# Kernel tuning notes

Measured on AMD Instinct MI355X. Metric: run time of the kernel, lower is better.

The kernel has to match this reference:

```python
import jax, jax.numpy as jnp
import numpy as np

B, T, N, D, H = 4, 8, 128, 256, 8
DH = D // H
SH_HID = 16
NUM_FEATS = 3
NUM_COEFF = 4  # l=0 (1) + l=1 (3)
Y0_CONST = 0.28209479177387814   # 1/(2*sqrt(pi)), e3nn 'integral' norm
Y1_CONST = 0.4886025119029199    # sqrt(3/(4*pi))


def setup_inputs() -> dict:
    key = jax.random.key(0)
    ks = jax.random.split(key, 16)
    rn = lambda k, shape, s=1.0: jax.random.normal(k, shape, dtype=jnp.float32) * s
    return {
        "x_0": rn(ks[0], (B, T, N, D)),
        "v_0": rn(ks[1], (B, T, N, D)),
        "concatenated_features": rn(ks[2], (B, T, N, D)),
        "q_data": rn(ks[3], (B, T, N, D)),
        "mask": jnp.ones((B, 1, N, 1), dtype=bool),
        "Wq": rn(ks[4], (D, D), 0.02), "bq": jnp.zeros((D,), jnp.float32),
        "Wkv": rn(ks[5], (NUM_FEATS, D, 2 * D), 0.02),
        "bkv": jnp.zeros((NUM_FEATS, 2 * D), jnp.float32),
        "Wo": rn(ks[6], (D, D), 0.02), "bo": jnp.zeros((D,), jnp.float32),
        "feature_weights": rn(ks[7], (NUM_FEATS,), 0.1),
        "attention_denom": jnp.full((H,), float(DH), dtype=jnp.float32),
        "sh_W1": rn(ks[8], (NUM_COEFF, SH_HID), 0.3), "sh_b1": jnp.zeros((SH_HID,), jnp.float32),
        "sh_W2": rn(ks[9], (SH_HID, SH_HID), 0.3), "sh_b2": jnp.zeros((SH_HID,), jnp.float32),
        "sh_W3": rn(ks[10], (SH_HID, H), 0.3), "sh_b3": jnp.zeros((H,), jnp.float32),
    }


def _rope(t, mask, T_, N_):
    # t: [B,H,S,dh]; time-only RoPE, groups of N_ nodes share a timestep. offset=0.
    B_, H_, S, dh = t.shape
    half = dh // 2
    freqs = 1.0 / (1000.0 ** (2.0 * jnp.arange(half, dtype=jnp.float32) / dh))  # [half]
    pos = jnp.repeat(jnp.arange(T_, dtype=jnp.float32), N_)  # [S]
    angle = pos[:, None] * freqs[None, :]  # [S, half]
    mask_seq = jnp.broadcast_to(mask, (B_, T_, N_, 1)).reshape(B_, 1, S, 1)
    cos_t = jnp.where(mask_seq, jnp.cos(angle)[None, None], 1.0)  # [B,1,S,half]
    sin_t = jnp.where(mask_seq, jnp.sin(angle)[None, None], 0.0)
    t1, t2 = t[..., 0::2], t[..., 1::2]
    return jnp.stack([t1 * cos_t - t2 * sin_t, t1 * sin_t + t2 * cos_t], axis=-1).reshape(t.shape)


def _sh_bias(coords, W1, b1, W2, b2, W3, b3):
    # coords: [B,S,3] -> bias [B,H,S,S]
    rel = coords[:, :, None, :] - coords[:, None, :, :]  # [B,S,S,3]
    norm = jnp.sqrt(jnp.sum(rel * rel, axis=-1, keepdims=True))
    u = rel / (norm + 1e-6)
    Y0 = jnp.full(u.shape[:-1] + (1,), Y0_CONST, dtype=u.dtype)
    Y1 = Y1_CONST * u[..., jnp.array([1, 2, 0])]  # e3nn l=1 order (y,z,x)
    sh = jnp.concatenate([Y0, Y1], axis=-1)  # [B,S,S,4]
    h = jax.nn.silu(sh @ W1 + b1)
    h = jax.nn.silu(h @ W2 + b2)
    bias = h @ W3 + b3  # [B,S,S,H]
    return jnp.transpose(bias, (0, 3, 1, 2))


def reference(x_0, v_0, concatenated_features, q_data, mask,
              Wq, bq, Wkv, bkv, Wo, bo, feature_weights, attention_denom,
              sh_W1, sh_b1, sh_W2, sh_b2, sh_W3, sh_b3):
    B_, T_, N_, D_ = q_data.shape
    S = T_ * N_
    H_ = attention_denom.shape[0]
    dh = D_ // H_

    q = (q_data.reshape(B_, S, D_) @ Wq + bq).reshape(B_, S, H_, dh).transpose(0, 2, 1, 3)
    q = _rope(q, mask, T_, N_)

    coords = x_0[..., :3].reshape(B_, S, 3)
    bias = _sh_bias(coords, sh_W1, sh_b1, sh_W2, sh_b2, sh_W3, sh_b3)  # [B,H,S,S]

    key_mask = jnp.broadcast_to(mask, (B_, T_, N_, 1)).reshape(B_, 1, 1, S)
    gates = jax.nn.softmax(feature_weights)

    out_sum = jnp.zeros_like(q)
    for i, feat in enumerate((x_0, v_0, concatenated_features)):
        kv = feat.reshape(B_, S, D_) @ Wkv[i] + bkv[i]  # [B,S,2D]
        k = kv[..., :D_].reshape(B_, S, H_, dh).transpose(0, 2, 1, 3)
        v = kv[..., D_:].reshape(B_, S, H_, dh).transpose(0, 2, 1, 3)
        k = _rope(k, mask, T_, N_)
        scores = jnp.einsum('bhqd,bhkd->bhqk', q, k) / attention_denom[None, :, None, None]
        scores = scores + bias
        scores = jnp.where(key_mask, scores, -1e9)
        attn = jax.nn.softmax(scores, axis=-1)
        out_sum = out_sum + gates[i] * jnp.einsum('bhqk,bhkd->bhqd', attn, v)

    out = out_sum.transpose(0, 2, 1, 3).reshape(B_, S, D_) @ Wo + bo  # [B,S,D]
    return out.reshape(B_ * T_, N_, D_)
```

## Files before the change

kernel.cpp:

```cpp
#include <hip/hip_runtime.h>
#include <hip/hip_bf16.h>
#include <math.h>


typedef __bf16 bf16;
typedef __attribute__((ext_vector_type(8))) __bf16 bf16x8;
typedef __attribute__((ext_vector_type(4))) __bf16 bf16x4;
typedef __attribute__((ext_vector_type(4))) float  f32x4;

#define MFMA16(a,b,c) __builtin_amdgcn_mfma_f32_16x16x32_bf16((a),(b),(c),0,0,0)
#define FRCP(x) __builtin_amdgcn_rcpf(x)

__global__ __launch_bounds__(256) void proj_kernel(
    const float* __restrict__ x0, const float* __restrict__ v0,
    const float* __restrict__ cf, const float* __restrict__ qd,
    const float* __restrict__ Wq, const float* __restrict__ bq,
    const float* __restrict__ Wkv, const float* __restrict__ bkv,
    const float* __restrict__ dn,
    bf16* __restrict__ Qb, bf16* __restrict__ Kb, bf16* __restrict__ Vtb)
{
  const int z  = blockIdx.z;
  const int mt = blockIdx.x;
  const int nt = blockIdx.y;
  if (z == 0 && nt >= 4) return;

  const float* A; const float* W; const float* bias; int ldw;
  if (z == 0){ A = qd; W = Wq; bias = bq; ldw = 256; }
  else {
    A = (z==1) ? x0 : (z==2) ? v0 : cf;
    W = Wkv + (size_t)(z-1)*256*512;
    bias = bkv + (size_t)(z-1)*512;
    ldw = 512;
  }

  __shared__ alignas(16) bf16 lds_a[64*264];
  __shared__ alignas(16) bf16 lds_w[64*264];
  const int t  = threadIdx.x;
  const int n0 = nt*64;

  #pragma unroll
  for (int i=0;i<16;i++){
    int flat = i*256 + t;
    int r = flat >> 6, c4 = flat & 63;
    float4 v = *(const float4*)(A + (size_t)(mt*64 + r)*256 + c4*4);
    bf16* dst = lds_a + r*264 + c4*4;
    dst[0]=(bf16)v.x; dst[1]=(bf16)v.y; dst[2]=(bf16)v.z; dst[3]=(bf16)v.w;
  }
  {
    int c4 = t & 15, kr = t >> 4;
    #pragma unroll
    for (int i=0;i<16;i++){
      int k = kr + i*16;
      float4 v = *(const float4*)(W + (size_t)k*ldw + n0 + c4*4);
      lds_w[(c4*4+0)*264 + k] = (bf16)v.x;
      lds_w[(c4*4+1)*264 + k] = (bf16)v.y;
      lds_w[(c4*4+2)*264 + k] = (bf16)v.z;
      lds_w[(c4*4+3)*264 + k] = (bf16)v.w;
    }
  }
  __syncthreads();

  const int w = t>>6, lane = t&63, lrow = lane&15, g = lane>>4;
  const f32x4 zf = {0.f,0.f,0.f,0.f};
  f32x4 acc[4] = {zf,zf,zf,zf};

  #pragma unroll
  for (int ks=0;ks<8;ks++){
    bf16x8 a = *(const bf16x8*)(lds_a + (w*16+lrow)*264 + ks*32 + g*8);
    #pragma unroll
    for (int n4=0;n4<4;n4++){
      bf16x8 bb = *(const bf16x8*)(lds_w + (n4*16+lrow)*264 + ks*32 + g*8);
      acc[n4] = MFMA16(a, bb, acc[n4]);
    }
  }

  const bool isV = (z>0) && (nt>=4);
  if (!isV){
    const float tpos = (float)((mt & 15) >> 1);
    const float Cln = 0.43172239f;
    float fr_e = __expf(-Cln * (float)(lrow>>1));
    float fr_o = __expf(-Cln * (float)(8 + (lrow>>1)));
    float ae = tpos*fr_e, ao = tpos*fr_o;
    float cs_e = __cosf(ae), sn_e = __sinf(ae);
    float cs_o = __cosf(ao), sn_o = __sinf(ao);
    float rs0 = 1.f, rs1 = 1.f;
    if (z==0){ rs0 = 1.f/dn[(nt*2)&7]; rs1 = 1.f/dn[(nt*2+1)&7]; }

    #pragma unroll
    for (int n4=0;n4<4;n4++){
      int gcol = n0 + n4*16 + lrow;
      float bv = bias[gcol];
      float cs = (n4&1)? cs_o : cs_e;
      float sn = (n4&1)? sn_o : sn_e;
      float rs = (n4>>1)? rs1 : rs0;
      #pragma unroll
      for (int rr=0;rr<4;rr++){
        float v = acc[n4][rr] + bv;
        float p = __shfl_xor(v, 1);
        float o = (lrow&1) ? (p*sn + v*cs) : (v*cs - p*sn);
        o *= rs;
        lds_a[(w*16 + g*4 + rr)*264 + n4*16 + lrow] = (bf16)o;
      }
    }
    int row = lane>>2, c8 = lane&3;
    int srow = mt*64 + w*16 + row;
    int bb = srow>>10, s = srow&1023;
    #pragma unroll
    for (int hh=0; hh<2; hh++){
      bf16x8 val = *(const bf16x8*)(lds_a + (w*16+row)*264 + hh*32 + c8*8);
      int h = (nt*2 + hh)&7;
      bf16* dst = (z==0) ? (Qb + ((size_t)(bb*8+h)*1024 + s)*32 + c8*8)
                         : (Kb + ((size_t)(((z-1)*4+bb)*8+h)*1024 + s)*32 + c8*8);
      *(bf16x8*)dst = val;
    }
  } else {
    #pragma unroll
    for (int n4=0;n4<4;n4++){
      int gcol = n0 + n4*16 + lrow;
      float bv = bias[gcol];
      int hd = gcol - 256; int h = hd>>5, d = hd&31;
      int grow0 = mt*64 + w*16 + g*4;
      int bb = grow0>>10, s0 = grow0&1023;
      int s0p = (s0 & ~31) | (((s0>>2)&3)<<3) | (((s0>>4)&1)<<2);
      bf16x4 pk;
      #pragma unroll
      for (int rr=0;rr<4;rr++) pk[rr] = (bf16)(acc[n4][rr] + bv);
      *(bf16x4*)(Vtb + (((size_t)((z-1)*4+bb)*8 + h)*32 + d)*1024 + s0p) = pk;
    }
  }
}

template<bool PART>
__global__ __launch_bounds__(512) void attn_kernel(
    const bf16* __restrict__ Qb, const bf16* __restrict__ Kb, const bf16* __restrict__ Vtb,
    const float* __restrict__ x0, const float* __restrict__ fw,
    const float* __restrict__ W1, const float* __restrict__ b1,
    const float* __restrict__ W2, const float* __restrict__ b2,
    const float* __restrict__ W3, const float* __restrict__ b3,
    float* __restrict__ osum, float* __restrict__ Pp, float* __restrict__ Lp)
{
  const int bid = blockIdx.x;
  const int xcd = bid & 7;
  const int b   = xcd >> 1;
  int qt, split;
  if (PART){ int r = bid>>3; qt = (xcd&1)*32 + (r&31); split = r>>5; }
  else     { qt = (xcd&1)*32 + (bid>>3); split = 0; }
  const int q0 = qt*16;
  constexpr int KTS = PART ? 8 : 16;
  constexpr int KC  = PART ? 512 : 1024;
  const int kbase = split*512;
  const int t = threadIdx.x, w = t>>6, lane = t&63, lrow = lane&15, g = lane>>4;

  __shared__ float ckA[KC][3];
  __shared__ float biasT[8*64*17];

  bf16x8 w1f, w2f, w3f;
  #pragma unroll
  for (int j=0;j<8;j++){
    w1f[j] = (g==0 && j<4)   ? (bf16)W1[j*16 + lrow]       : (bf16)0.f;
    w2f[j] = (j<4)           ? (bf16)W2[(4*g+j)*16 + lrow] : (bf16)0.f;
    w3f[j] = (j<4 && lrow<8) ? (bf16)W3[(4*g+j)*8 + lrow]  : (bf16)0.f;
  }
  float b1r[4], b2r[4], b3r[4];
  #pragma unroll
  for (int rr=0;rr<4;rr++){
    b1r[rr] = b1[g*4+rr];
    b2r[rr] = b2[g*4+rr];
    b3r[rr] = (g<2) ? b3[g*4+rr] : 0.f;
  }

  bf16x8 qf = *(const bf16x8*)(Qb + (((size_t)(b*8+w)*1024) + q0 + lrow)*32 + g*8);

  #pragma unroll
  for (int u=0; u<KC/512; u++){
    int key = u*512 + t;
    const float* src = x0 + ((size_t)b*1024 + kbase + key)*256;
    ckA[key][0] = src[0]; ckA[key][1] = src[1]; ckA[key][2] = src[2];
  }
  const float* qsrc = x0 + ((size_t)b*1024 + q0 + lrow)*256;
  const float cqx = qsrc[0], cqy = qsrc[1], cqz = qsrc[2];
  __syncthreads();

  float l_run[3] = {0.f,0.f,0.f};
  const f32x4 zf = {0.f,0.f,0.f,0.f};
  f32x4 acc[3][2];
  #pragma unroll
  for (int i=0;i<3;i++){ acc[i][0] = zf; acc[i][1] = zf; }

  for (int kt=0;kt<KTS;kt++){
    const int k0 = kt*64;
    const int kg = kbase + k0;

    #pragma unroll
    for (int m8=0;m8<8;m8++){
      const int m = w*8 + m8;
      float rx = cqx - ckA[k0+m][0];
      float ry = cqy - ckA[k0+m][1];
      float rz = cqz - ckA[k0+m][2];
      float inv = FRCP(__builtin_amdgcn_sqrtf(rx*rx+ry*ry+rz*rz) + 1e-6f);
      bf16x8 shf;
      #pragma unroll
      for (int j=0;j<8;j++) shf[j] = (bf16)0.f;
      if (g==0){
        shf[0] = (bf16)0.28209479177387814f;
        shf[1] = (bf16)(0.4886025119029199f*ry*inv);
        shf[2] = (bf16)(0.4886025119029199f*rz*inv);
        shf[3] = (bf16)(0.4886025119029199f*rx*inv);
      }
      f32x4 c1 = MFMA16(w1f, shf, zf);
      bf16x8 h1f;
      #pragma unroll
      for (int rr=0;rr<4;rr++){
        float hv = c1[rr] + b1r[rr];
        hv = hv * FRCP(1.f + __expf(-hv));
        bf16 hb = (bf16)hv;
        h1f[rr] = hb; h1f[rr+4] = hb;
      }
      f32x4 c2 = MFMA16(w2f, h1f, zf);
      bf16x8 h2f;
      #pragma unroll
      for (int rr=0;rr<4;rr++){
        float hv = c2[rr] + b2r[rr];
        hv = hv * FRCP(1.f + __expf(-hv));
        bf16 hb = (bf16)hv;
        h2f[rr] = hb; h2f[rr+4] = hb;
      }
      f32x4 c3 = MFMA16(w3f, h2f, zf);
      if (g < 2){
        #pragma unroll
        for (int rr=0;rr<4;rr++)
          biasT[((g*4+rr)*64 + m)*17 + lrow] = c3[rr] + b3r[rr];
      }
    }
    __syncthreads();

    float bias_r[4][4];
    #pragma unroll
    for (int k16=0;k16<4;k16++)
      #pragma unroll
      for (int rr=0;rr<4;rr++)
        bias_r[k16][rr] = biasT[(w*64 + k16*16 + g*4 + rr)*17 + lrow];

    #pragma unroll
    for (int i=0;i<3;i++){
      const bf16* Kbase = Kb + ((size_t)(i*4+b)*8 + w)*1024*32;
      float p[4][4];
      float ls = 0.f;
      #pragma unroll
      for (int k16=0;k16<4;k16++){
        bf16x8 kf = *(const bf16x8*)(Kbase + (size_t)(kg + k16*16 + lrow)*32 + g*8);
        f32x4 sc = MFMA16(kf, qf, zf);
        #pragma unroll
        for (int rr=0;rr<4;rr++){
          float pv = __expf(sc[rr] + bias_r[k16][rr]);
          p[k16][rr] = pv;
          ls += pv;
        }
      }
      l_run[i] += ls;
      bf16x8 pf0, pf1;
      #pragma unroll
      for (int j=0;j<8;j++){
        pf0[j] = (bf16)p[(j>>2)][j&3];
        pf1[j] = (bf16)p[2+(j>>2)][j&3];
      }
      const bf16* Vbase = Vtb + ((size_t)(i*4+b)*8 + w)*32*1024;
      #pragma unroll
      for (int dt=0;dt<2;dt++){
        bf16x8 vf0 = *(const bf16x8*)(Vbase + (size_t)(dt*16+lrow)*1024 + kg      + g*8);
        bf16x8 vf1 = *(const bf16x8*)(Vbase + (size_t)(dt*16+lrow)*1024 + kg + 32 + g*8);
        acc[i][dt] = MFMA16(vf0, pf0, acc[i][dt]);
        acc[i][dt] = MFMA16(vf1, pf1, acc[i][dt]);
      }
    }
    __syncthreads();
  }

  if (PART){
    #pragma unroll
    for (int i=0;i<3;i++){
      float l = l_run[i];
      l += __shfl_xor(l, 16);
      l += __shfl_xor(l, 32);
      if (lane < 16)
        Lp[((size_t)(i*2+split)*4+b)*8192 + w*1024 + q0 + lrow] = l;
      #pragma unroll
      for (int dt=0;dt<2;dt++)
        *(f32x4*)(Pp + (((size_t)(i*2+split)*4 + b)*1024 + q0 + lrow)*256
                     + w*32 + dt*16 + g*4) = acc[i][dt];
    }
  } else {
    float f0=fw[0], f1=fw[1], f2=fw[2];
    float fm = fmaxf(f0, fmaxf(f1,f2));
    float e0=__expf(f0-fm), e1=__expf(f1-fm), e2=__expf(f2-fm);
    float ei = FRCP(e0+e1+e2);
    float gate[3] = {e0*ei, e1*ei, e2*ei};
    float linv[3];
    #pragma unroll
    for (int i=0;i<3;i++){
      float l = l_run[i];
      l += __shfl_xor(l, 16);
      l += __shfl_xor(l, 32);
      linv[i] = gate[i]*FRCP(l);
    }
    #pragma unroll
    for (int dt=0;dt<2;dt++){
      f32x4 o;
      #pragma unroll
      for (int rr=0;rr<4;rr++)
        o[rr] = acc[0][dt][rr]*linv[0] + acc[1][dt][rr]*linv[1] + acc[2][dt][rr]*linv[2];
      *(f32x4*)(osum + ((size_t)b*1024 + q0 + lrow)*256 + w*32 + dt*16 + g*4) = o;
    }
  }
}

__global__ __launch_bounds__(256) void combine_kernel(
    const float* __restrict__ Pp, const float* __restrict__ Lp,
    const float* __restrict__ fw, float* __restrict__ osum)
{
  int idx  = blockIdx.x*256 + threadIdx.x;
  int col4 = idx & 63;
  int row  = idx >> 6;
  int b = row >> 10, q = row & 1023;
  int h = col4 >> 3;
  float f0=fw[0], f1=fw[1], f2=fw[2];
  float fm = fmaxf(f0, fmaxf(f1,f2));
  float e0=__expf(f0-fm), e1=__expf(f1-fm), e2=__expf(f2-fm);
  float ei = 1.f/(e0+e1+e2);
  float gate[3] = {e0*ei, e1*ei, e2*ei};
  f32x4 o = {0.f,0.f,0.f,0.f};
  #pragma unroll
  for (int i=0;i<3;i++){
    f32x4 a = ((const f32x4*)Pp)[(((size_t)(i*2+0)*4 + b)*1024 + q)*64 + col4];
    f32x4 c = ((const f32x4*)Pp)[(((size_t)(i*2+1)*4 + b)*1024 + q)*64 + col4];
    float l = Lp[((size_t)(i*2+0)*4+b)*8192 + h*1024 + q]
            + Lp[((size_t)(i*2+1)*4+b)*8192 + h*1024 + q];
    float s = gate[i]/l;
    #pragma unroll
    for (int rr=0;rr<4;rr++) o[rr] += (a[rr]+c[rr])*s;
  }
  ((f32x4*)osum)[idx] = o;
}

__global__ __launch_bounds__(256) void oproj_kernel(
    const float* __restrict__ As, const float* __restrict__ Wo,
    const float* __restrict__ bo, float* __restrict__ out)
{
  const int mt = blockIdx.x, nt = blockIdx.y;
  __shared__ alignas(16) bf16 lds_a[64*264];
  __shared__ alignas(16) bf16 lds_w[64*264];
  const int t = threadIdx.x;
  const int n0 = nt*64;
  #pragma unroll
  for (int i=0;i<16;i++){
    int flat = i*256 + t;
    int r = flat >> 6, c4 = flat & 63;
    float4 v = *(const float4*)(As + (size_t)(mt*64 + r)*256 + c4*4);
    bf16* dst = lds_a + r*264 + c4*4;
    dst[0]=(bf16)v.x; dst[1]=(bf16)v.y; dst[2]=(bf16)v.z; dst[3]=(bf16)v.w;
  }
  {
    int c4 = t & 15, kr = t >> 4;
    #pragma unroll
    for (int i=0;i<16;i++){
      int k = kr + i*16;
      float4 v = *(const float4*)(Wo + (size_t)k*256 + n0 + c4*4);
      lds_w[(c4*4+0)*264 + k] = (bf16)v.x;
      lds_w[(c4*4+1)*264 + k] = (bf16)v.y;
      lds_w[(c4*4+2)*264 + k] = (bf16)v.z;
      lds_w[(c4*4+3)*264 + k] = (bf16)v.w;
    }
  }
  __syncthreads();
  const int w = t>>6, lane = t&63, lrow = lane&15, g = lane>>4;
  const f32x4 zf = {0.f,0.f,0.f,0.f};
  f32x4 acc[4] = {zf,zf,zf,zf};
  #pragma unroll
  for (int ks=0;ks<8;ks++){
    bf16x8 a = *(const bf16x8*)(lds_a + (w*16+lrow)*264 + ks*32 + g*8);
    #pragma unroll
    for (int n4=0;n4<4;n4++){
      bf16x8 bb = *(const bf16x8*)(lds_w + (n4*16+lrow)*264 + ks*32 + g*8);
      acc[n4] = MFMA16(a, bb, acc[n4]);
    }
  }
  #pragma unroll
  for (int n4=0;n4<4;n4++){
    int gcol = n0 + n4*16 + lrow;
    float bv = bo[gcol];
    #pragma unroll
    for (int rr=0;rr<4;rr++){
      int grow = mt*64 + w*16 + g*4 + rr;
      out[(size_t)grow*256 + gcol] = acc[n4][rr] + bv;
    }
  }
}

extern "C" void kernel_launch(void* const* d_in, const int* in_sizes, int n_in,
                              void* d_out, int out_size, void* d_ws, size_t ws_size,
                              hipStream_t stream)
{
  (void)in_sizes; (void)n_in; (void)out_size;
  const float* x0 = (const float*)d_in[0];
  const float* v0 = (const float*)d_in[1];
  const float* cf = (const float*)d_in[2];
  const float* qd = (const float*)d_in[3];
  const float* Wq = (const float*)d_in[5];
  const float* bq = (const float*)d_in[6];
  const float* Wkv= (const float*)d_in[7];
  const float* bkv= (const float*)d_in[8];
  const float* Wo = (const float*)d_in[9];
  const float* bo = (const float*)d_in[10];
  const float* fw = (const float*)d_in[11];
  const float* dn = (const float*)d_in[12];
  const float* W1 = (const float*)d_in[13];
  const float* b1 = (const float*)d_in[14];
  const float* W2 = (const float*)d_in[15];
  const float* b2 = (const float*)d_in[16];
  const float* W3 = (const float*)d_in[17];
  const float* b3 = (const float*)d_in[18];

  const size_t nQ = (size_t)4*8*1024*32;
  const size_t nK = (size_t)3*4*8*1024*32;
  bf16*  Qb   = (bf16*)d_ws;
  bf16*  Kb   = Qb + nQ;
  bf16*  Vtb  = Kb + nK;
  float* osum = (float*)(Vtb + nK);
  float* Pp   = osum + (size_t)4*1024*256;
  float* Lp   = Pp + (size_t)3*2*4*1024*256;
  const size_t need_part = (nQ + 2*nK)*2
                         + ((size_t)4*1024*256 + (size_t)3*2*4*1024*256 + (size_t)3*2*4*8*1024)*4;
  float* outp = (float*)d_out;

  hipLaunchKernelGGL(proj_kernel, dim3(64,8,4), dim3(256), 0, stream,
                     x0, v0, cf, qd, Wq, bq, Wkv, bkv, dn, Qb, Kb, Vtb);
  if (ws_size >= need_part){
    hipLaunchKernelGGL((attn_kernel<true>), dim3(512), dim3(512), 0, stream,
                       Qb, Kb, Vtb, x0, fw, W1,b1,W2,b2,W3,b3, osum, Pp, Lp);
    hipLaunchKernelGGL(combine_kernel, dim3(1024), dim3(256), 0, stream,
                       Pp, Lp, fw, osum);
  } else {
    hipLaunchKernelGGL((attn_kernel<false>), dim3(256), dim3(512), 0, stream,
                       Qb, Kb, Vtb, x0, fw, W1,b1,W2,b2,W3,b3, osum, Pp, Lp);
  }
  hipLaunchKernelGGL(oproj_kernel, dim3(64,4), dim3(256), 0, stream,
                     osum, Wo, bo, outp);
}
```

Before: 260.3 us.

## Merge key-split attention into one 1024-thread block and rework projection grid

The attention key split now runs inside a single 1024-thread block, with two wave groups each covering half the keys. The partial results are merged through shared memory, which removes the Pp/Lp global partial buffers and the separate combine kernel launch. The projection kernel drops its idle z=0 blocks with a compact 16x28 grid. Each projection block now loops over 4 M-tiles while reusing the staged weight tile, and A is read directly from global memory into registers instead of through LDS. Risks include lower occupancy from the 1024-thread blocks and larger shared memory use, fewer blocks in the projection kernel, and uncoalesced direct loads of A.

Result: slower. 278.4 us (+7.0%).

```diff
diff --git a/kernel.cpp b/kernel.cpp
--- a/kernel.cpp
+++ b/kernel.cpp
@@ -19,10 +19,10 @@
     const float* __restrict__ dn,
     bf16* __restrict__ Qb, bf16* __restrict__ Kb, bf16* __restrict__ Vtb)
 {
-  const int z  = blockIdx.z;
-  const int mt = blockIdx.x;
-  const int nt = blockIdx.y;
-  if (z == 0 && nt >= 4) return;
+  const int mtc = blockIdx.x;
+  const int znt = blockIdx.y;
+  int z, nt;
+  if (znt < 4){ z = 0; nt = znt; } else { z = 1 + ((znt-4)>>3); nt = (znt-4)&7; }
 
   const float* A; const float* W; const float* bias; int ldw;
   if (z == 0){ A = qd; W = Wq; bias = bq; ldw = 256; }
@@ -33,19 +33,11 @@
     ldw = 512;
   }
 
-  __shared__ alignas(16) bf16 lds_a[64*264];
   __shared__ alignas(16) bf16 lds_w[64*264];
+  __shared__ alignas(16) bf16 ostg[4][1152];
   const int t  = threadIdx.x;
   const int n0 = nt*64;
 
-  #pragma unroll
-  for (int i=0;i<16;i++){
-    int flat = i*256 + t;
-    int r = flat >> 6, c4 = flat & 63;
-    float4 v = *(const float4*)(A + (size_t)(mt*64 + r)*256 + c4*4);
-    bf16* dst = lds_a + r*264 + c4*4;
-    dst[0]=(bf16)v.x; dst[1]=(bf16)v.y; dst[2]=(bf16)v.z; dst[3]=(bf16)v.w;
-  }
   {
     int c4 = t & 15, kr = t >> 4;
     #pragma unroll
@@ -62,97 +54,104 @@
 
   const int w = t>>6, lane = t&63, lrow = lane&15, g = lane>>4;
   const f32x4 zf = {0.f,0.f,0.f,0.f};
-  f32x4 acc[4] = {zf,zf,zf,zf};
-
-  #pragma unroll
-  for (int ks=0;ks<8;ks++){
-    bf16x8 a = *(const bf16x8*)(lds_a + (w*16+lrow)*264 + ks*32 + g*8);
-    #pragma unroll
-    for (int n4=0;n4<4;n4++){
-      bf16x8 bb = *(const bf16x8*)(lds_w + (n4*16+lrow)*264 + ks*32 + g*8);
-      acc[n4] = MFMA16(a, bb, acc[n4]);
-    }
-  }
-
   const bool isV = (z>0) && (nt>=4);
-  if (!isV){
-    const float tpos = (float)((mt & 15) >> 1);
-    const float Cln = 0.43172239f;
-    float fr_e = __expf(-Cln * (float)(lrow>>1));
-    float fr_o = __expf(-Cln * (float)(8 + (lrow>>1)));
-    float ae = tpos*fr_e, ao = tpos*fr_o;
-    float cs_e = __cosf(ae), sn_e = __sinf(ae);
-    float cs_o = __cosf(ao), sn_o = __sinf(ao);
-    float rs0 = 1.f, rs1 = 1.f;
-    if (z==0){ rs0 = 1.f/dn[(nt*2)&7]; rs1 = 1.f/dn[(nt*2+1)&7]; }
-
-    #pragma unroll
-    for (int n4=0;n4<4;n4++){
-      int gcol = n0 + n4*16 + lrow;
-      float bv = bias[gcol];
-      float cs = (n4&1)? cs_o : cs_e;
-      float sn = (n4&1)? sn_o : sn_e;
-      float rs = (n4>>1)? rs1 : rs0;
-      #pragma unroll
-      for (int rr=0;rr<4;rr++){
-        float v = acc[n4][rr] + bv;
-        float p = __shfl_xor(v, 1);
-        float o = (lrow&1) ? (p*sn + v*cs) : (v*cs - p*sn);
-        o *= rs;
-        lds_a[(w*16 + g*4 + rr)*264 + n4*16 + lrow] = (bf16)o;
-      }
-    }
-    int row = lane>>2, c8 = lane&3;
-    int srow = mt*64 + w*16 + row;
-    int bb = srow>>10, s = srow&1023;
-    #pragma unroll
-    for (int hh=0; hh<2; hh++){
-      bf16x8 val = *(const bf16x8*)(lds_a + (w*16+row)*264 + hh*32 + c8*8);
-      int h = (nt*2 + hh)&7;
-      bf16* dst = (z==0) ? (Qb + ((size_t)(bb*8+h)*1024 + s)*32 + c8*8)
-                         : (Kb + ((size_t)(((z-1)*4+bb)*8+h)*1024 + s)*32 + c8*8);
-      *(bf16x8*)dst = val;
-    }
-  } else {
-    #pragma unroll
-    for (int n4=0;n4<4;n4++){
-      int gcol = n0 + n4*16 + lrow;
-      float bv = bias[gcol];
-      int hd = gcol - 256; int h = hd>>5, d = hd&31;
-      int grow0 = mt*64 + w*16 + g*4;
-      int bb = grow0>>10, s0 = grow0&1023;
-      int s0p = (s0 & ~31) | (((s0>>2)&3)<<3) | (((s0>>4)&1)<<2);
-      bf16x4 pk;
-      #pragma unroll
-      for (int rr=0;rr<4;rr++) pk[rr] = (bf16)(acc[n4][rr] + bv);
-      *(bf16x4*)(Vtb + (((size_t)((z-1)*4+bb)*8 + h)*32 + d)*1024 + s0p) = pk;
+
+  const float Cln = 0.43172239f;
+  const float fr_e = __expf(-Cln * (float)(lrow>>1));
+  const float fr_o = __expf(-Cln * (float)(8 + (lrow>>1)));
+  float rs0 = 1.f, rs1 = 1.f;
+  if (z==0){ rs0 = 1.f/dn[(nt*2)&7]; rs1 = 1.f/dn[(nt*2+1)&7]; }
+
+  for (int mi=0; mi<4; mi++){
+    const int mt = mtc*4 + mi;
+    const float* Arow = A + (size_t)(mt*64 + w*16 + lrow)*256;
+
+    f32x4 acc[4] = {zf,zf,zf,zf};
+    #pragma unroll
+    for (int ks=0;ks<8;ks++){
+      float4 a0 = *(const float4*)(Arow + ks*32 + g*8);
+      float4 a1 = *(const float4*)(Arow + ks*32 + g*8 + 4);
+      bf16x8 af = {(bf16)a0.x,(bf16)a0.y,(bf16)a0.z,(bf16)a0.w,
+                   (bf16)a1.x,(bf16)a1.y,(bf16)a1.z,(bf16)a1.w};
+      #pragma unroll
+      for (int n4=0;n4<4;n4++){
+        bf16x8 bb = *(const bf16x8*)(lds_w + (n4*16+lrow)*264 + ks*32 + g*8);
+        acc[n4] = MFMA16(af, bb, acc[n4]);
+      }
+    }
+
+    if (!isV){
+      const float tpos = (float)((mt>>1)&7);
+      float ae = tpos*fr_e, ao = tpos*fr_o;
+      float cs_e = __cosf(ae), sn_e = __sinf(ae);
+      float cs_o = __cosf(ao), sn_o = __sinf(ao);
+      #pragma unroll
+      for (int n4=0;n4<4;n4++){
+        int gcol = n0 + n4*16 + lrow;
+        float bv = bias[gcol];
+        float cs = (n4&1)? cs_o : cs_e;
+        float sn = (n4&1)? sn_o : sn_e;
+        float rs = (n4>>1)? rs1 : rs0;
+        #pragma unroll
+        for (int rr=0;rr<4;rr++){
+          float v = acc[n4][rr] + bv;
+          float p = __shfl_xor(v, 1);
+          float o = (lrow&1) ? (p*sn + v*cs) : (v*cs - p*sn);
+          o *= rs;
+          ostg[w][(g*4+rr)*72 + n4*16 + lrow] = (bf16)o;
+        }
+      }
+      asm volatile("s_waitcnt lgkmcnt(0)" ::: "memory");
+      int row = lane>>2, c8 = lane&3;
+      int srow = mt*64 + w*16 + row;
+      int bb = srow>>10, s = srow&1023;
+      #pragma unroll
+      for (int hh=0; hh<2; hh++){
+        bf16x8 val = *(const bf16x8*)(ostg[w] + row*72 + hh*32 + c8*8);
+        int h = (nt*2 + hh)&7;
+        bf16* dst = (z==0) ? (Qb + ((size_t)(bb*8+h)*1024 + s)*32 + c8*8)
+                           : (Kb + ((size_t)(((z-1)*4+bb)*8+h)*1024 + s)*32 + c8*8);
+        *(bf16x8*)dst = val;
+      }
+    } else {
+      #pragma unroll
+      for (int n4=0;n4<4;n4++){
+        int gcol = n0 + n4*16 + lrow;
+        float bv = bias[gcol];
+        int hd = gcol - 256; int h = hd>>5, d = hd&31;
+        int grow0 = mt*64 + w*16 + g*4;
+        int bb = grow0>>10, s0 = grow0&1023;
+        int s0p = (s0 & ~31) | (((s0>>2)&3)<<3) | (((s0>>4)&1)<<2);
+        bf16x4 pk;
+        #pragma unroll
+        for (int rr=0;rr<4;rr++) pk[rr] = (bf16)(acc[n4][rr] + bv);
+        *(bf16x4*)(Vtb + (((size_t)((z-1)*4+bb)*8 + h)*32 + d)*1024 + s0p) = pk;
+      }
     }
   }
 }
 
-template<bool PART>
-__global__ __launch_bounds__(512) void attn_kernel(
+__global__ __launch_bounds__(1024) void attn_kernel(
     const bf16* __restrict__ Qb, const bf16* __restrict__ Kb, const bf16* __restrict__ Vtb,
     const float* __restrict__ x0, const float* __restrict__ fw,
     const float* __restrict__ W1, const float* __restrict__ b1,
     const float* __restrict__ W2, const float* __restrict__ b2,
     const float* __restrict__ W3, const float* __restrict__ b3,
-    float* __restrict__ osum, float* __restrict__ Pp, float* __restrict__ Lp)
+    float* __restrict__ osum)
 {
   const int bid = blockIdx.x;
   const int xcd = bid & 7;
   const int b   = xcd >> 1;
-  int qt, split;
-  if (PART){ int r = bid>>3; qt = (xcd&1)*32 + (r&31); split = r>>5; }
-  else     { qt = (xcd&1)*32 + (bid>>3); split = 0; }
-  const int q0 = qt*16;
-  constexpr int KTS = PART ? 8 : 16;
-  constexpr int KC  = PART ? 512 : 1024;
+  const int qt  = (xcd & 1)*32 + (bid >> 3);
+  const int q0  = qt*16;
+  const int t = threadIdx.x;
+  const int w16 = t>>6, split = w16>>3, w = w16&7;
+  const int lane = t&63, lrow = lane&15, g = lane>>4;
   const int kbase = split*512;
-  const int t = threadIdx.x, w = t>>6, lane = t&63, lrow = lane&15, g = lane>>4;
-
-  __shared__ float ckA[KC][3];
-  __shared__ float biasT[8*64*17];
+
+  __shared__ float smem[20480];
+  float* ckA = smem;
+  float* bT  = smem + 3072 + split*8704;
 
   bf16x8 w1f, w2f, w3f;
   #pragma unroll
@@ -171,15 +170,12 @@
 
   bf16x8 qf = *(const bf16x8*)(Qb + (((size_t)(b*8+w)*1024) + q0 + lrow)*32 + g*8);
 
-  #pragma unroll
-  for (int u=0; u<KC/512; u++){
-    int key = u*512 + t;
-    const float* src = x0 + ((size_t)b*1024 + kbase + key)*256;
-    ckA[key][0] = src[0]; ckA[key][1] = src[1]; ckA[key][2] = src[2];
-  }
-  const float* qsrc = x0 + ((size_t)b*1024 + q0 + lrow)*256;
-  const float cqx = qsrc[0], cqy = qsrc[1], cqz = qsrc[2];
+  {
+    const float* src = x0 + ((size_t)b*1024 + t)*256;
+    ckA[t*3+0] = src[0]; ckA[t*3+1] = src[1]; ckA[t*3+2] = src[2];
+  }
   __syncthreads();
+  const float cqx = ckA[(q0+lrow)*3+0], cqy = ckA[(q0+lrow)*3+1], cqz = ckA[(q0+lrow)*3+2];
 
   float l_run[3] = {0.f,0.f,0.f};
   const f32x4 zf = {0.f,0.f,0.f,0.f};
@@ -187,16 +183,15 @@
   #pragma unroll
   for (int i=0;i<3;i++){ acc[i][0] = zf; acc[i][1] = zf; }
 
-  for (int kt=0;kt<KTS;kt++){
-    const int k0 = kt*64;
-    const int kg = kbase + k0;
+  for (int kt=0;kt<8;kt++){
+    const int kg = kbase + kt*64;
 
     #pragma unroll
     for (int m8=0;m8<8;m8++){
       const int m = w*8 + m8;
-      float rx = cqx - ckA[k0+m][0];
-      float ry = cqy - ckA[k0+m][1];
-      float rz = cqz - ckA[k0+m][2];
+      float rx = cqx - ckA[(kg+m)*3+0];
+      float ry = cqy - ckA[(kg+m)*3+1];
+      float rz = cqz - ckA[(kg+m)*3+2];
       float inv = FRCP(__builtin_amdgcn_sqrtf(rx*rx+ry*ry+rz*rz) + 1e-6f);
       bf16x8 shf;
       #pragma unroll
@@ -229,7 +224,7 @@
       if (g < 2){
         #pragma unroll
         for (int rr=0;rr<4;rr++)
-          biasT[((g*4+rr)*64 + m)*17 + lrow] = c3[rr] + b3r[rr];
+          bT[((g*4+rr)*64 + m)*17 + lrow] = c3[rr] + b3r[rr];
       }
     }
     __syncthreads();
@@ -239,7 +234,7 @@
     for (int k16=0;k16<4;k16++)
       #pragma unroll
       for (int rr=0;rr<4;rr++)
-        bias_r[k16][rr] = biasT[(w*64 + k16*16 + g*4 + rr)*17 + lrow];
+        bias_r[k16][rr] = bT[(w*64 + k16*16 + g*4 + rr)*17 + lrow];
 
     #pragma unroll
     for (int i=0;i<3;i++){
@@ -276,20 +271,28 @@
     __syncthreads();
   }
 
-  if (PART){
+  if (split == 1){
+    float* mb = smem + (w*64 + lane)*28;
     #pragma unroll
     for (int i=0;i<3;i++){
-      float l = l_run[i];
-      l += __shfl_xor(l, 16);
-      l += __shfl_xor(l, 32);
-      if (lane < 16)
-        Lp[((size_t)(i*2+split)*4+b)*8192 + w*1024 + q0 + lrow] = l;
       #pragma unroll
       for (int dt=0;dt<2;dt++)
-        *(f32x4*)(Pp + (((size_t)(i*2+split)*4 + b)*1024 + q0 + lrow)*256
-                     + w*32 + dt*16 + g*4) = acc[i][dt];
-    }
-  } else {
+        #pragma unroll
+        for (int rr=0;rr<4;rr++) mb[i*8 + dt*4 + rr] = acc[i][dt][rr];
+      mb[24+i] = l_run[i];
+    }
+  }
+  __syncthreads();
+  if (split == 0){
+    float* mb = smem + (w*64 + lane)*28;
+    #pragma unroll
+    for (int i=0;i<3;i++){
+      #pragma unroll
+      for (int dt=0;dt<2;dt++)
+        #pragma unroll
+        for (int rr=0;rr<4;rr++) acc[i][dt][rr] += mb[i*8 + dt*4 + rr];
+      l_run[i] += mb[24+i];
+    }
     float f0=fw[0], f1=fw[1], f2=fw[2];
     float fm = fmaxf(f0, fmaxf(f1,f2));
     float e0=__expf(f0-fm), e1=__expf(f1-fm), e2=__expf(f2-fm);
@@ -312,34 +315,6 @@
       *(f32x4*)(osum + ((size_t)b*1024 + q0 + lrow)*256 + w*32 + dt*16 + g*4) = o;
     }
   }
-}
-
-__global__ __launch_bounds__(256) void combine_kernel(
-    const float* __restrict__ Pp, const float* __restrict__ Lp,
-    const float* __restrict__ fw, float* __restrict__ osum)
-{
-  int idx  = blockIdx.x*256 + threadIdx.x;
-  int col4 = idx & 63;
-  int row  = idx >> 6;
-  int b = row >> 10, q = row & 1023;
-  int h = col4 >> 3;
-  float f0=fw[0], f1=fw[1], f2=fw[2];
-  float fm = fmaxf(f0, fmaxf(f1,f2));
-  float e0=__expf(f0-fm), e1=__expf(f1-fm), e2=__expf(f2-fm);
-  float ei = 1.f/(e0+e1+e2);
-  float gate[3] = {e0*ei, e1*ei, e2*ei};
-  f32x4 o = {0.f,0.f,0.f,0.f};
-  #pragma unroll
-  for (int i=0;i<3;i++){
-    f32x4 a = ((const f32x4*)Pp)[(((size_t)(i*2+0)*4 + b)*1024 + q)*64 + col4];
-    f32x4 c = ((const f32x4*)Pp)[(((size_t)(i*2+1)*4 + b)*1024 + q)*64 + col4];
-    float l = Lp[((size_t)(i*2+0)*4+b)*8192 + h*1024 + q]
-            + Lp[((size_t)(i*2+1)*4+b)*8192 + h*1024 + q];
-    float s = gate[i]/l;
-    #pragma unroll
-    for (int rr=0;rr<4;rr++) o[rr] += (a[rr]+c[rr])*s;
-  }
-  ((f32x4*)osum)[idx] = o;
 }
 
 __global__ __launch_bounds__(256) void oproj_kernel(
@@ -400,7 +375,7 @@
                               void* d_out, int out_size, void* d_ws, size_t ws_size,
                               hipStream_t stream)
 {
-  (void)in_sizes; (void)n_in; (void)out_size;
+  (void)in_sizes; (void)n_in; (void)out_size; (void)ws_size;
   const float* x0 = (const float*)d_in[0];
   const float* v0 = (const float*)d_in[1];
   const float* cf = (const float*)d_in[2];
@@ -426,23 +401,12 @@
   bf16*  Kb   = Qb + nQ;
   bf16*  Vtb  = Kb + nK;
   float* osum = (float*)(Vtb + nK);
-  float* Pp   = osum + (size_t)4*1024*256;
-  float* Lp   = Pp + (size_t)3*2*4*1024*256;
-  const size_t need_part = (nQ + 2*nK)*2
-                         + ((size_t)4*1024*256 + (size_t)3*2*4*1024*256 + (size_t)3*2*4*8*1024)*4;
   float* outp = (float*)d_out;
 
-  hipLaunchKernelGGL(proj_kernel, dim3(64,8,4), dim3(256), 0, stream,
+  hipLaunchKernelGGL(proj_kernel, dim3(16,28), dim3(256), 0, stream,
                      x0, v0, cf, qd, Wq, bq, Wkv, bkv, dn, Qb, Kb, Vtb);
-  if (ws_size >= need_part){
-    hipLaunchKernelGGL((attn_kernel<true>), dim3(512), dim3(512), 0, stream,
-                       Qb, Kb, Vtb, x0, fw, W1,b1,W2,b2,W3,b3, osum, Pp, Lp);
-    hipLaunchKernelGGL(combine_kernel, dim3(1024), dim3(256), 0, stream,
-                       Pp, Lp, fw, osum);
-  } else {
-    hipLaunchKernelGGL((attn_kernel<false>), dim3(256), dim3(512), 0, stream,
-                       Qb, Kb, Vtb, x0, fw, W1,b1,W2,b2,W3,b3, osum, Pp, Lp);
-  }
+  hipLaunchKernelGGL(attn_kernel, dim3(256), dim3(1024), 0, stream,
+                     Qb, Kb, Vtb, x0, fw, W1,b1,W2,b2,W3,b3, osum);
   hipLaunchKernelGGL(oproj_kernel, dim3(64,4), dim3(256), 0, stream,
                      osum, Wo, bo, outp);
 }
```
